# Optimization experiments

Measured on AMD Instinct MI355X. Metric: run time of the kernel, lower is better.

## Reference

```python
import jax, jax.numpy as jnp
import numpy as np

EPS = 1e-8

def setup_inputs() -> dict:
    key = jax.random.key(0)
    ks = jax.random.split(key, 8)
    b, s, d, E = 8, 2048, 512, 8
    queries = jax.random.normal(ks[0], (b, s, d), dtype=jnp.float32)
    keys = jax.random.normal(ks[1], (b, s, d), dtype=jnp.float32)
    # learned parameters (match torch init scales; randomize strengths/orientations
    # so entry-point contributions are nonzero/active-mixed)
    center = jax.random.normal(ks[2], (d,), dtype=jnp.float32) * 0.02
    outer_radius = jnp.asarray(1.0, dtype=jnp.float32)
    hole_radius = jnp.asarray(0.01, dtype=jnp.float32)
    entry_points = jax.random.normal(ks[3], (E, d), dtype=jnp.float32) * 0.1
    entry_strengths = jax.random.normal(ks[4], (E,), dtype=jnp.float32) * 1.0 + 0.3
    entry_orientations = jax.random.normal(ks[5], (E,), dtype=jnp.float32) * 0.5
    return {"queries": queries, "keys": keys, "center": center,
            "outer_radius": outer_radius, "hole_radius": hole_radius,
            "entry_points": entry_points, "entry_strengths": entry_strengths,
            "entry_orientations": entry_orientations}

def _surface_weights(dists, outer_radius, hole_ratio):
    # gaussian branch (hole_ratio < 0.05) vs torus-shell branch
    gauss = jnp.exp(-0.5 * (dists / (outer_radius + EPS)) ** 2)
    torus = jnp.exp(-0.5 * jnp.abs(dists - outer_radius) ** 2)
    return jnp.where(hole_ratio < 0.05, gauss, torus)

def _entry_sqdists(x, pts):
    # squared euclidean distance x:[b,s,d] vs pts:[E,d] -> [b,s,E]
    x2 = jnp.sum(x * x, axis=-1, keepdims=True)          # [b,s,1]
    p2 = jnp.sum(pts * pts, axis=-1)                     # [E]
    xp = jnp.einsum('bsd,ed->bse', x, pts)               # [b,s,E]
    return jnp.maximum(x2 + p2 - 2.0 * xp, 0.0)

def reference(queries, keys, center, outer_radius, hole_radius,
              entry_points, entry_strengths, entry_orientations):
    # distances to torus center
    q_dists = jnp.linalg.norm(queries - center, axis=-1)   # [b,s]
    k_dists = jnp.linalg.norm(keys - center, axis=-1)      # [b,s]
    hole_ratio = hole_radius / (outer_radius + EPS)
    qw = _surface_weights(q_dists, outer_radius, hole_ratio)
    kw = _surface_weights(k_dists, outer_radius, hole_ratio)
    surface = jnp.einsum('bi,bj->bij', qw, kw)             # rank-1 outer product
    # entry-point contributions: cdist^2 -> gaussian weights -> low-rank sum
    strengths = jax.nn.sigmoid(entry_strengths)            # [E]
    coef = jnp.where(strengths > 0.3, strengths * jnp.tanh(entry_orientations), 0.0)
    eqw = jnp.exp(-0.5 * _entry_sqdists(queries, entry_points))  # [b,s,E]
    ekw = jnp.exp(-0.5 * _entry_sqdists(keys, entry_points))     # [b,s,E]
    entry = jnp.einsum('bie,e,bje->bij', eqw, coef, ekw)
    return surface + entry
```

## Files before the change

### kernel.cpp

```cpp
#include <hip/hip_runtime.h>

#define EPSF 1e-8f

__device__ __forceinline__ float wave_reduce_sum(float v) {
#pragma unroll
    for (int m = 32; m >= 1; m >>= 1)
        v += __shfl_xor(v, m, 64);
    return v;
}

__device__ __forceinline__ float sq8(const float4& xa, const float4& xb,
                                     const float4& pa, const float4& pb) {
    float t, a = 0.f;
    t = xa.x - pa.x; a = fmaf(t, t, a);
    t = xa.y - pa.y; a = fmaf(t, t, a);
    t = xa.z - pa.z; a = fmaf(t, t, a);
    t = xa.w - pa.w; a = fmaf(t, t, a);
    t = xb.x - pb.x; a = fmaf(t, t, a);
    t = xb.y - pb.y; a = fmaf(t, t, a);
    t = xb.z - pb.z; a = fmaf(t, t, a);
    t = xb.w - pb.w; a = fmaf(t, t, a);
    return a;
}

__global__ __launch_bounds__(256) void feat_kernel(
    const float* __restrict__ q, const float* __restrict__ k,
    const float* __restrict__ center,
    const float* __restrict__ outer_radius_p,
    const float* __restrict__ hole_radius_p,
    const float* __restrict__ entry_points,
    const float* __restrict__ strengths_p,
    const float* __restrict__ orientations_p,
    float* __restrict__ U, float* __restrict__ V, int NR)
{
    const int gid  = blockIdx.x * blockDim.x + threadIdx.x;
    const int wave = gid >> 6;
    const int lane = gid & 63;
    const bool is_key = wave >= NR;
    const int row = is_key ? wave - NR : wave;

    const float* x = (is_key ? k : q) + (size_t)row * 512 + lane * 8;
    const float4 xa = ((const float4*)x)[0];
    const float4 xb = ((const float4*)x)[1];

    const float* c = center + lane * 8;
    const float4 ca = ((const float4*)c)[0];
    const float4 cb = ((const float4*)c)[1];

    float acc[9];
    acc[0] = sq8(xa, xb, ca, cb);

#pragma unroll
    for (int e = 0; e < 8; e++) {
        const float* p = entry_points + e * 512 + lane * 8;
        const float4 pa = ((const float4*)p)[0];
        const float4 pb = ((const float4*)p)[1];
        acc[1 + e] = sq8(xa, xb, pa, pb);
    }

#pragma unroll
    for (int r = 0; r < 9; r++) acc[r] = wave_reduce_sum(acc[r]);

    if (lane == 0) {
        const float R  = outer_radius_p[0];
        const float hr = hole_radius_p[0] / (R + EPSF);
        const float dist = sqrtf(acc[0]);
        float w;
        if (hr < 0.05f) {
            const float td = dist / (R + EPSF);
            w = expf(-0.5f * td * td);
        } else {
            const float td = fabsf(dist - R);
            w = expf(-0.5f * td * td);
        }
        float* O = is_key ? V : U;
        O[row] = w;
#pragma unroll
        for (int e = 0; e < 8; e++) {
            float we = expf(-0.5f * acc[1 + e]);
            if (!is_key) {
                const float st = 1.f / (1.f + expf(-strengths_p[e]));
                const float cf = (st > 0.3f) ? st * tanhf(orientations_p[e]) : 0.f;
                we *= cf;
            }
            O[(size_t)(1 + e) * NR + row] = we;
        }
    }
}

__global__ __launch_bounds__(256) void outer_kernel(
    const float* __restrict__ U, const float* __restrict__ V,
    float* __restrict__ out, int s, int NR)
{
    const int b = blockIdx.z;
    const int i = blockIdx.y;
    const int j = (blockIdx.x * 256 + threadIdx.x) * 4;
    const int rowU = b * s + i;
    const int rowV = b * s + j;

    float u[9];
#pragma unroll
    for (int r = 0; r < 9; r++) u[r] = U[(size_t)r * NR + rowU];

    float4 acc = make_float4(0.f, 0.f, 0.f, 0.f);
#pragma unroll
    for (int r = 0; r < 9; r++) {
        const float4 v = *(const float4*)(V + (size_t)r * NR + rowV);
        acc.x = fmaf(u[r], v.x, acc.x);
        acc.y = fmaf(u[r], v.y, acc.y);
        acc.z = fmaf(u[r], v.z, acc.z);
        acc.w = fmaf(u[r], v.w, acc.w);
    }
    *(float4*)(out + (size_t)rowU * s + j) = acc;
}

extern "C" void kernel_launch(void* const* d_in, const int* in_sizes, int n_in,
                              void* d_out, int out_size, void* d_ws, size_t ws_size,
                              hipStream_t stream) {
    const float* q        = (const float*)d_in[0];
    const float* k        = (const float*)d_in[1];
    const float* center   = (const float*)d_in[2];
    const float* outer_r  = (const float*)d_in[3];
    const float* hole_r   = (const float*)d_in[4];
    const float* entry_p  = (const float*)d_in[5];
    const float* strengths    = (const float*)d_in[6];
    const float* orientations = (const float*)d_in[7];

    const int d  = 512;
    const int NR = in_sizes[0] / d;
    const int s  = (int)((long long)out_size / NR);
    const int b  = NR / s;

    float* U = (float*)d_ws;
    float* V = U + (size_t)9 * NR;

    const int threads1 = 256;
    const int blocks1  = (2 * NR * 64) / threads1;
    feat_kernel<<<blocks1, threads1, 0, stream>>>(
        q, k, center, outer_r, hole_r, entry_p, strengths, orientations, U, V, NR);

    dim3 g2(s / (256 * 4), s, b);
    outer_kernel<<<g2, 256, 0, stream>>>(U, V, (float*)d_out, s, NR);
}
```

Before: 225.3 us.

## Tile outer-product kernel over 16 query rows to reuse V loads

```diff
diff --git a/kernel.cpp b/kernel.cpp
--- a/kernel.cpp
+++ b/kernel.cpp
@@ -88,30 +88,44 @@
     }
 }
 
+#define TILE_I 16
 __global__ __launch_bounds__(256) void outer_kernel(
     const float* __restrict__ U, const float* __restrict__ V,
     float* __restrict__ out, int s, int NR)
 {
-    const int b = blockIdx.z;
-    const int i = blockIdx.y;
-    const int j = (blockIdx.x * 256 + threadIdx.x) * 4;
-    const int rowU = b * s + i;
+    const int b  = blockIdx.z;
+    const int i0 = blockIdx.y * TILE_I;
+    const int j  = (blockIdx.x * 256 + threadIdx.x) * 4;
+
+    __shared__ float u_s[9][TILE_I];
+    if (threadIdx.x < 9 * TILE_I) {
+        const int r  = threadIdx.x / TILE_I;
+        const int ii = threadIdx.x % TILE_I;
+        u_s[r][ii] = U[(size_t)r * NR + b * s + i0 + ii];
+    }
+
+    float4 v[9];
     const int rowV = b * s + j;
+#pragma unroll
+    for (int r = 0; r < 9; r++)
+        v[r] = *(const float4*)(V + (size_t)r * NR + rowV);
 
-    float u[9];
+    __syncthreads();
+
+    float* orow = out + ((size_t)(b * s + i0)) * s + j;
 #pragma unroll
-    for (int r = 0; r < 9; r++) u[r] = U[(size_t)r * NR + rowU];
-
-    float4 acc = make_float4(0.f, 0.f, 0.f, 0.f);
+    for (int ii = 0; ii < TILE_I; ii++) {
+        float4 acc = make_float4(0.f, 0.f, 0.f, 0.f);
 #pragma unroll
-    for (int r = 0; r < 9; r++) {
-        const float4 v = *(const float4*)(V + (size_t)r * NR + rowV);
-        acc.x = fmaf(u[r], v.x, acc.x);
-        acc.y = fmaf(u[r], v.y, acc.y);
-        acc.z = fmaf(u[r], v.z, acc.z);
-        acc.w = fmaf(u[r], v.w, acc.w);
+        for (int r = 0; r < 9; r++) {
+            const float ur = u_s[r][ii];
+            acc.x = fmaf(ur, v[r].x, acc.x);
+            acc.y = fmaf(ur, v[r].y, acc.y);
+            acc.z = fmaf(ur, v[r].z, acc.z);
+            acc.w = fmaf(ur, v[r].w, acc.w);
+        }
+        *(float4*)(orow + (size_t)ii * s) = acc;
     }
-    *(float4*)(out + (size_t)rowU * s + j) = acc;
 }
 
 extern "C" void kernel_launch(void* const* d_in, const int* in_sizes, int n_in,
@@ -139,6 +153,6 @@
     feat_kernel<<<blocks1, threads1, 0, stream>>>(
         q, k, center, outer_r, hole_r, entry_p, strengths, orientations, U, V, NR);
 
-    dim3 g2(s / (256 * 4), s, b);
+    dim3 g2(s / (256 * 4), s / TILE_I, b);
     outer_kernel<<<g2, 256, 0, stream>>>(U, V, (float*)d_out, s, NR);
 }
```

Result: faster. 211.2 us, median of 2 (-6.3%).
